# Kernel optimization log

Hardware: AMD Instinct MI355X
Metric: run time of the kernel (lower is better)

Reference implementation:

```python
import jax, jax.numpy as jnp
import numpy as np

B, T, D, H = 16, 4096, 256, 512  # batch, seq_len, ninputs, nhiddens


def setup_inputs() -> dict:
    key = jax.random.key(0)
    k_x, k_ih, k_hh, k_b, k_bn = jax.random.split(key, 5)
    s = 1.0 / np.sqrt(H)
    xs = jax.random.normal(k_x, (B, T, D), dtype=jnp.float32)
    W_ih = jax.random.uniform(k_ih, (3 * H, D), minval=-s, maxval=s, dtype=jnp.float32)
    W_hh = jax.random.uniform(k_hh, (3 * H, H), minval=-s, maxval=s, dtype=jnp.float32)
    b = jax.random.uniform(k_b, (3 * H,), minval=-s, maxval=s, dtype=jnp.float32)
    b_n = jax.random.uniform(k_bn, (H,), minval=-s, maxval=s, dtype=jnp.float32)
    return {"xs": xs, "W_ih": W_ih, "W_hh": W_hh, "b": b, "b_n": b_n}


def _gru_scan(xs, W_ih, W_hh, b, b_n):
    # Precompute all input-side gates with one big GEMM: (B, T, 3H)
    igates = jnp.einsum('btd,gd->btg', xs, W_ih) + b

    def step(h, ig):
        # h: (B, H), ig: (B, 3H)
        hg = h @ W_hh.T  # (B, 3H)
        i_r, i_z, i_n = jnp.split(ig, 3, axis=-1)
        h_r, h_z, h_n = jnp.split(hg, 3, axis=-1)
        r = jax.nn.sigmoid(i_r + h_r)   # reset gate
        z = jax.nn.sigmoid(i_z + h_z)   # update gate (equinox 'inp')
        n = jnp.tanh(i_n + r * (h_n + b_n))
        h_new = n + z * (h - n)         # equinox: new + inp * (hidden - new)
        return h_new, h_new

    h0 = jnp.zeros((xs.shape[0], b_n.shape[0]), dtype=xs.dtype)
    _, ys = jax.lax.scan(step, h0, jnp.swapaxes(igates, 0, 1))  # (T, B, H)
    return jnp.swapaxes(ys, 0, 1)  # (B, T, H)


def reference(xs, W_ih, W_hh, b, b_n):
    # CellLayer('gru', 'deer') computes the exact GRU recurrence over time
    # (DEER's fixed point equals the sequential evaluation).
    return _gru_scan(xs, W_ih, W_hh, b, b_n)
```

## Files before the change

### kernel.cpp

```cpp
#include <hip/hip_runtime.h>
#include <stdint.h>
#include <stddef.h>

#define B_ 16
#define T_ 4096
#define D_ 256
#define H_ 512
#define G3_ 1536

#define OFF_IG   ((size_t)0)
#define OFF_WT   ((size_t)201326592)
#define OFF_MB   ((size_t)202899456)
#define WS_NEED  ((size_t)203161600)

typedef _Float16 h2_t __attribute__((ext_vector_type(2)));

#if defined(__has_builtin)
#if __has_builtin(__builtin_amdgcn_fdot2)
#define HAVE_FDOT2 1
#endif
#endif

__device__ __forceinline__ float fdot2f(uint32_t w, uint32_t h, float acc) {
  union { uint32_t u; h2_t v; } a, b;
  a.u = w; b.u = h;
#ifdef HAVE_FDOT2
  return __builtin_amdgcn_fdot2(a.v, b.v, acc, false);
#else
  return fmaf((float)a.v.x, (float)b.v.x, fmaf((float)a.v.y, (float)b.v.y, acc));
#endif
}

__device__ __forceinline__ uint32_t packh2(float a, float b) {
  union { h2_t v; uint32_t u; } x;
  x.v.x = (_Float16)a; x.v.y = (_Float16)b;
  return x.u;
}

__device__ __forceinline__ uint32_t f16bits(float a) {
  union { _Float16 h; uint16_t u; } x;
  x.h = (_Float16)a;
  return (uint32_t)x.u;
}

__device__ __forceinline__ float h2f(uint16_t u) {
  union { _Float16 h; uint16_t u; } x;
  x.u = u;
  return (float)x.h;
}

__device__ __forceinline__ float sigmoidf_(float x) {
  return 1.0f / (1.0f + __expf(-x));
}

__device__ __forceinline__ float tanhf_(float x) {
  x = fminf(fmaxf(x, -15.0f), 15.0f);
  float e = __expf(-2.0f * x);
  return (1.0f - e) / (1.0f + e);
}

__global__ void __launch_bounds__(256) wt_kernel(const float* __restrict__ W, float4* __restrict__ Wt4) {
  int idx = blockIdx.x * 256 + threadIdx.x;
  if (idx >= G3_ * 64) return;
  int g = idx % G3_;
  int d4 = idx / G3_;
  float4 v = *(const float4*)(W + (size_t)g * D_ + 4 * d4);
  Wt4[(size_t)d4 * G3_ + g] = v;
}

__global__ void __launch_bounds__(256) ig_kernel(const float* __restrict__ xs,
                                                 const float* __restrict__ Wt,
                                                 const float* __restrict__ bias,
                                                 _Float16* __restrict__ ig) {
  __shared__ float xls[16 * 256];
  const int m0 = blockIdx.x * 16;
  const int tid = threadIdx.x;

  const float4* xsrc = (const float4*)(xs + (size_t)m0 * D_);
  float4* xdst = (float4*)xls;
#pragma unroll
  for (int k = 0; k < 4; ++k) xdst[tid + 256 * k] = xsrc[tid + 256 * k];
  __syncthreads();

  float acc[6][16];
#pragma unroll
  for (int k = 0; k < 6; ++k)
#pragma unroll
    for (int m = 0; m < 16; ++m) acc[k][m] = 0.0f;

  const float4* Wt4 = (const float4*)Wt;
  const float4* lds4 = (const float4*)xls;

  for (int d4 = 0; d4 < 64; ++d4) {
    float4 w[6];
#pragma unroll
    for (int k = 0; k < 6; ++k) w[k] = Wt4[(size_t)d4 * G3_ + tid + 256 * k];
#pragma unroll
    for (int m = 0; m < 16; ++m) {
      float4 xv = lds4[m * 64 + d4];
#pragma unroll
      for (int k = 0; k < 6; ++k) {
        acc[k][m] = fmaf(w[k].x, xv.x, acc[k][m]);
        acc[k][m] = fmaf(w[k].y, xv.y, acc[k][m]);
        acc[k][m] = fmaf(w[k].z, xv.z, acc[k][m]);
        acc[k][m] = fmaf(w[k].w, xv.w, acc[k][m]);
      }
    }
  }

#pragma unroll
  for (int k = 0; k < 6; ++k) {
    float bb = bias[tid + 256 * k];
#pragma unroll
    for (int m = 0; m < 16; ++m) {
      ig[(size_t)(m0 + m) * G3_ + tid + 256 * k] = (_Float16)(acc[k][m] + bb);
    }
  }
}

__global__ void __launch_bounds__(256, 1) rec_kernel(const _Float16* __restrict__ ig,
                                                     const float* __restrict__ Whh,
                                                     const float* __restrict__ bn,
                                                     uint32_t* __restrict__ mb,
                                                     float* __restrict__ out) {
  const int wg = blockIdx.x;
  const int b = wg >> 3;
  const int sub = wg & 7;
  const int tid = threadIdx.x;
  const int q = tid & 3;
  const int cl = tid >> 2;
  const int j = sub * 64 + cl;

  uint32_t wr[64], wz[64], wn[64];
  {
    const float4* s0 = (const float4*)(Whh + (size_t)j * H_ + q * 128);
    const float4* s1 = (const float4*)(Whh + (size_t)(j + H_) * H_ + q * 128);
    const float4* s2 = (const float4*)(Whh + (size_t)(j + 2 * H_) * H_ + q * 128);
#pragma unroll
    for (int i = 0; i < 32; ++i) {
      float4 v0 = s0[i]; wr[2 * i] = packh2(v0.x, v0.y); wr[2 * i + 1] = packh2(v0.z, v0.w);
      float4 v1 = s1[i]; wz[2 * i] = packh2(v1.x, v1.y); wz[2 * i + 1] = packh2(v1.z, v1.w);
      float4 v2 = s2[i]; wn[2 * i] = packh2(v2.x, v2.y); wn[2 * i + 1] = packh2(v2.z, v2.w);
    }
  }
  const float bnj = bn[j];

  __shared__ uint32_t hl[4 * 68];
  for (int i = tid; i < 4 * 68; i += 256) hl[i] = 0;
  __syncthreads();

  float hprev = 0.0f;

  const size_t mb_bc = ((size_t)b * 8 + sub) * 512;
  const size_t par_stride = (size_t)B_ * 8 * 512;
  const size_t dst0 = ((size_t)b * 8 + q) * 512 + (size_t)j;
  const size_t dst1 = ((size_t)b * 8 + (q + 4)) * 512 + (size_t)j;

  const uint16_t* ig16 = (const uint16_t*)ig;
  size_t igbase = (size_t)b * T_ * G3_;

  uint16_t cr = ig16[igbase + j];
  uint16_t cz = ig16[igbase + j + H_];
  uint16_t cn = ig16[igbase + j + 2 * H_];

  for (int t = 0; t < T_; ++t) {
    uint16_t nr = 0, nz = 0, nn_ = 0;
    if (t + 1 < T_) {
      const size_t nb = igbase + G3_;
      nr = ig16[nb + j];
      nz = ig16[nb + j + H_];
      nn_ = ig16[nb + j + 2 * H_];
    }

    if (t > 0) {
      const uint32_t* pb = mb + (size_t)(t & 1) * par_stride + mb_bc;
      const int k0 = 2 * tid;
      const uint32_t want = (uint32_t)t;
      uint32_t v0 = 0, v1 = 0;
      bool d0 = false, d1 = false;
      int guard = 0;
      for (;;) {
        uint32_t a0 = 0, a1 = 0;
        if (!d0) a0 = __hip_atomic_load(&pb[k0], __ATOMIC_RELAXED, __HIP_MEMORY_SCOPE_AGENT);
        if (!d1) a1 = __hip_atomic_load(&pb[k0 + 1], __ATOMIC_RELAXED, __HIP_MEMORY_SCOPE_AGENT);
        if (!d0 && (a0 >> 16) == want) { v0 = a0; d0 = true; }
        if (!d1 && (a1 >> 16) == want) { v1 = a1; d1 = true; }
        if (d0 && d1) break;
        if (++guard > 65536) {
          if (!d0) v0 = 0x7C00u;
          if (!d1) v1 = 0x7C00u;
          break;
        }
      }
      hl[(tid >> 6) * 68 + (tid & 63)] = (v0 & 0xFFFFu) | (v1 << 16);
      __syncthreads();
    }

    float ar0 = 0.0f, az0 = 0.0f, an0 = 0.0f;
    float ar1 = 0.0f, az1 = 0.0f, an1 = 0.0f;
    const uint4* hq = (const uint4*)(&hl[q * 68]);
#pragma unroll
    for (int i = 0; i < 8; ++i) {
      uint4 hv = hq[i];
      ar0 = fdot2f(wr[4 * i + 0], hv.x, ar0); az0 = fdot2f(wz[4 * i + 0], hv.x, az0); an0 = fdot2f(wn[4 * i + 0], hv.x, an0);
      ar0 = fdot2f(wr[4 * i + 1], hv.y, ar0); az0 = fdot2f(wz[4 * i + 1], hv.y, az0); an0 = fdot2f(wn[4 * i + 1], hv.y, an0);
      ar0 = fdot2f(wr[4 * i + 2], hv.z, ar0); az0 = fdot2f(wz[4 * i + 2], hv.z, az0); an0 = fdot2f(wn[4 * i + 2], hv.z, an0);
      ar0 = fdot2f(wr[4 * i + 3], hv.w, ar0); az0 = fdot2f(wz[4 * i + 3], hv.w, az0); an0 = fdot2f(wn[4 * i + 3], hv.w, an0);
    }
#pragma unroll
    for (int i = 8; i < 16; ++i) {
      uint4 hv = hq[i];
      ar1 = fdot2f(wr[4 * i + 0], hv.x, ar1); az1 = fdot2f(wz[4 * i + 0], hv.x, az1); an1 = fdot2f(wn[4 * i + 0], hv.x, an1);
      ar1 = fdot2f(wr[4 * i + 1], hv.y, ar1); az1 = fdot2f(wz[4 * i + 1], hv.y, az1); an1 = fdot2f(wn[4 * i + 1], hv.y, an1);
      ar1 = fdot2f(wr[4 * i + 2], hv.z, ar1); az1 = fdot2f(wz[4 * i + 2], hv.z, az1); an1 = fdot2f(wn[4 * i + 2], hv.z, an1);
      ar1 = fdot2f(wr[4 * i + 3], hv.w, ar1); az1 = fdot2f(wz[4 * i + 3], hv.w, an1 == an1 ? az1 : az1); an1 = fdot2f(wn[4 * i + 3], hv.w, an1);
    }
    __syncthreads();

    float ar = ar0 + ar1, az = az0 + az1, an = an0 + an1;
    ar += __shfl_xor(ar, 1); ar += __shfl_xor(ar, 2);
    az += __shfl_xor(az, 1); az += __shfl_xor(az, 2);
    an += __shfl_xor(an, 1); an += __shfl_xor(an, 2);

    const float igr = h2f(cr), igz = h2f(cz), ign = h2f(cn);
    const float r = sigmoidf_(igr + ar);
    const float z = sigmoidf_(igz + az);
    const float n = tanhf_(ign + r * (an + bnj));
    const float hnew = n + z * (hprev - n);
    hprev = hnew;

    const uint32_t wv = ((uint32_t)(t + 1) << 16) | f16bits(hnew);
    uint32_t* nbuf = mb + (size_t)((t + 1) & 1) * par_stride;
    __hip_atomic_store(&nbuf[dst0], wv, __ATOMIC_RELAXED, __HIP_MEMORY_SCOPE_AGENT);
    __hip_atomic_store(&nbuf[dst1], wv, __ATOMIC_RELAXED, __HIP_MEMORY_SCOPE_AGENT);

    if (q == 0) {
      out[((size_t)b * T_ + t) * H_ + j] = hnew;
    }

    cr = nr; cz = nz; cn = nn_;
    igbase += G3_;
  }
}

__global__ void __launch_bounds__(512) naive_kernel(const float* __restrict__ xs,
                                                    const float* __restrict__ Wih,
                                                    const float* __restrict__ Whh,
                                                    const float* __restrict__ bias,
                                                    const float* __restrict__ bn,
                                                    float* __restrict__ out) {
  const int b = blockIdx.x;
  const int j = threadIdx.x;
  __shared__ float h[H_];
  __shared__ float xr[D_];
  h[j] = 0.0f;
  __syncthreads();
  for (int t = 0; t < T_; ++t) {
    if (j < D_) xr[j] = xs[((size_t)b * T_ + t) * D_ + j];
    __syncthreads();
    float a[2];
#pragma unroll
    for (int g = 0; g < 2; ++g) {
      const int row = j + g * H_;
      float s = bias[row];
      const float* wi = Wih + (size_t)row * D_;
      for (int d = 0; d < D_; ++d) s = fmaf(wi[d], xr[d], s);
      const float* wh = Whh + (size_t)row * H_;
      for (int k = 0; k < H_; ++k) s = fmaf(wh[k], h[k], s);
      a[g] = s;
    }
    const float r = sigmoidf_(a[0]);
    const float z = sigmoidf_(a[1]);
    float i_n = bias[j + 2 * H_];
    {
      const float* wi = Wih + (size_t)(j + 2 * H_) * D_;
      for (int d = 0; d < D_; ++d) i_n = fmaf(wi[d], xr[d], i_n);
    }
    float h_n = 0.0f;
    {
      const float* wh = Whh + (size_t)(j + 2 * H_) * H_;
      for (int k = 0; k < H_; ++k) h_n = fmaf(wh[k], h[k], h_n);
    }
    const float nn = tanhf_(i_n + r * (h_n + bn[j]));
    const float hnew = nn + z * (h[j] - nn);
    __syncthreads();
    h[j] = hnew;
    out[((size_t)b * T_ + t) * H_ + j] = hnew;
  }
}

extern "C" void kernel_launch(void* const* d_in, const int* in_sizes, int n_in,
                              void* d_out, int out_size, void* d_ws, size_t ws_size,
                              hipStream_t stream) {
  const float* xs  = (const float*)d_in[0];
  const float* Wih = (const float*)d_in[1];
  const float* Whh = (const float*)d_in[2];
  const float* bia = (const float*)d_in[3];
  const float* bnp = (const float*)d_in[4];
  float* out = (float*)d_out;

  if (ws_size >= WS_NEED) {
    char* ws = (char*)d_ws;
    _Float16* igp = (_Float16*)(ws + OFF_IG);
    float* wtp = (float*)(ws + OFF_WT);
    uint32_t* mbp = (uint32_t*)(ws + OFF_MB);

    hipMemsetAsync(mbp, 0, 2 * B_ * 8 * 512 * sizeof(uint32_t), stream);

    wt_kernel<<<dim3(384), dim3(256), 0, stream>>>(Wih, (float4*)wtp);
    ig_kernel<<<dim3((B_ * T_) / 16), dim3(256), 0, stream>>>(xs, wtp, bia, igp);
    rec_kernel<<<dim3(128), dim3(256), 0, stream>>>(igp, Whh, bnp, mbp, out);
  } else {
    naive_kernel<<<dim3(B_), dim3(H_), 0, stream>>>(xs, Wih, Whh, bia, bnp, out);
  }
}
```

Baseline: 8.927 ms.

## Use sc0 polling loads, double-buffer shared h, remap workgroups across XCDs

The spin-wait on the per-step mailbox now uses inline-asm global loads with the sc0 cache bit instead of agent-scope atomic loads, with a fallback to the old atomic loop if polling exceeds a bound. Shared hidden-state staging is double-buffered by step parity, which removes one __syncthreads per timestep. Workgroup-to-(batch, sub) mapping is permuted so the eight slices of one batch land on the same XCD under round-robin dispatch, keeping mailbox traffic within one L2. The risks are relying on sc0 loads for cross-workgroup coherence and the single-barrier ordering.

```diff
diff --git a/kernel.cpp b/kernel.cpp
--- a/kernel.cpp
+++ b/kernel.cpp
@@ -59,6 +59,16 @@
   return (1.0f - e) / (1.0f + e);
 }
 
+__device__ __forceinline__ void load2_sc0(const uint32_t* p0, const uint32_t* p1,
+                                          uint32_t& a0, uint32_t& a1) {
+  asm volatile("global_load_dword %0, %2, off sc0\n\t"
+               "global_load_dword %1, %3, off sc0\n\t"
+               "s_waitcnt vmcnt(0)"
+               : "=&v"(a0), "=&v"(a1)
+               : "v"(p0), "v"(p1)
+               : "memory");
+}
+
 __global__ void __launch_bounds__(256) wt_kernel(const float* __restrict__ W, float4* __restrict__ Wt4) {
   int idx = blockIdx.x * 256 + threadIdx.x;
   if (idx >= G3_ * 64) return;
@@ -124,8 +134,10 @@
                                                      uint32_t* __restrict__ mb,
                                                      float* __restrict__ out) {
   const int wg = blockIdx.x;
-  const int b = wg >> 3;
-  const int sub = wg & 7;
+  const int c = wg & 7;
+  const int m_ = wg >> 3;
+  const int b = c + 8 * (m_ & 1);
+  const int sub = m_ >> 1;
   const int tid = threadIdx.x;
   const int q = tid & 3;
   const int cl = tid >> 2;
@@ -145,60 +157,72 @@
   }
   const float bnj = bn[j];
 
-  __shared__ uint32_t hl[4 * 68];
-  for (int i = tid; i < 4 * 68; i += 256) hl[i] = 0;
+  __shared__ uint32_t hl[2][4 * 68];
+  for (int i = tid; i < 2 * 4 * 68; i += 256) ((uint32_t*)hl)[i] = 0;
   __syncthreads();
 
   float hprev = 0.0f;
-
+  bool fast = true;
+
+  const size_t par_stride = (size_t)B_ * 8 * 512;
   const size_t mb_bc = ((size_t)b * 8 + sub) * 512;
-  const size_t par_stride = (size_t)B_ * 8 * 512;
   const size_t dst0 = ((size_t)b * 8 + q) * 512 + (size_t)j;
   const size_t dst1 = ((size_t)b * 8 + (q + 4)) * 512 + (size_t)j;
 
   const uint16_t* ig16 = (const uint16_t*)ig;
   size_t igbase = (size_t)b * T_ * G3_;
-
   uint16_t cr = ig16[igbase + j];
   uint16_t cz = ig16[igbase + j + H_];
   uint16_t cn = ig16[igbase + j + 2 * H_];
 
   for (int t = 0; t < T_; ++t) {
-    uint16_t nr = 0, nz = 0, nn_ = 0;
+    uint16_t nr = 0, nz = 0, nn2 = 0;
     if (t + 1 < T_) {
       const size_t nb = igbase + G3_;
       nr = ig16[nb + j];
       nz = ig16[nb + j + H_];
-      nn_ = ig16[nb + j + 2 * H_];
+      nn2 = ig16[nb + j + 2 * H_];
     }
 
     if (t > 0) {
-      const uint32_t* pb = mb + (size_t)(t & 1) * par_stride + mb_bc;
+      uint32_t* pb = mb + (size_t)(t & 1) * par_stride + mb_bc;
       const int k0 = 2 * tid;
       const uint32_t want = (uint32_t)t;
       uint32_t v0 = 0, v1 = 0;
       bool d0 = false, d1 = false;
-      int guard = 0;
-      for (;;) {
-        uint32_t a0 = 0, a1 = 0;
-        if (!d0) a0 = __hip_atomic_load(&pb[k0], __ATOMIC_RELAXED, __HIP_MEMORY_SCOPE_AGENT);
-        if (!d1) a1 = __hip_atomic_load(&pb[k0 + 1], __ATOMIC_RELAXED, __HIP_MEMORY_SCOPE_AGENT);
-        if (!d0 && (a0 >> 16) == want) { v0 = a0; d0 = true; }
-        if (!d1 && (a1 >> 16) == want) { v1 = a1; d1 = true; }
-        if (d0 && d1) break;
-        if (++guard > 65536) {
-          if (!d0) v0 = 0x7C00u;
-          if (!d1) v1 = 0x7C00u;
-          break;
+
+      if (fast) {
+        for (int g = 0; g < 4096; ++g) {
+          uint32_t a0, a1;
+          load2_sc0(&pb[k0], &pb[k0 + 1], a0, a1);
+          if (!d0 && (a0 >> 16) == want) { v0 = a0; d0 = true; }
+          if (!d1 && (a1 >> 16) == want) { v1 = a1; d1 = true; }
+          if (d0 && d1) break;
+        }
+        if (!(d0 && d1)) fast = false;
+      }
+      if (!(d0 && d1)) {
+        int guard = 0;
+        for (;;) {
+          uint32_t a0 = __hip_atomic_load(&pb[k0], __ATOMIC_RELAXED, __HIP_MEMORY_SCOPE_AGENT);
+          uint32_t a1 = __hip_atomic_load(&pb[k0 + 1], __ATOMIC_RELAXED, __HIP_MEMORY_SCOPE_AGENT);
+          if (!d0 && (a0 >> 16) == want) { v0 = a0; d0 = true; }
+          if (!d1 && (a1 >> 16) == want) { v1 = a1; d1 = true; }
+          if (d0 && d1) break;
+          if (++guard > (1 << 20)) {
+            if (!d0) v0 = 0x7C00u;
+            if (!d1) v1 = 0x7C00u;
+            break;
+          }
         }
       }
-      hl[(tid >> 6) * 68 + (tid & 63)] = (v0 & 0xFFFFu) | (v1 << 16);
-      __syncthreads();
-    }
-
+      hl[t & 1][(tid >> 6) * 68 + (tid & 63)] = (v0 & 0xFFFFu) | (v1 << 16);
+    }
+    __syncthreads();
+
+    const uint4* hq = (const uint4*)(&hl[t & 1][q * 68]);
     float ar0 = 0.0f, az0 = 0.0f, an0 = 0.0f;
     float ar1 = 0.0f, az1 = 0.0f, an1 = 0.0f;
-    const uint4* hq = (const uint4*)(&hl[q * 68]);
 #pragma unroll
     for (int i = 0; i < 8; ++i) {
       uint4 hv = hq[i];
@@ -213,9 +237,8 @@
       ar1 = fdot2f(wr[4 * i + 0], hv.x, ar1); az1 = fdot2f(wz[4 * i + 0], hv.x, az1); an1 = fdot2f(wn[4 * i + 0], hv.x, an1);
       ar1 = fdot2f(wr[4 * i + 1], hv.y, ar1); az1 = fdot2f(wz[4 * i + 1], hv.y, az1); an1 = fdot2f(wn[4 * i + 1], hv.y, an1);
       ar1 = fdot2f(wr[4 * i + 2], hv.z, ar1); az1 = fdot2f(wz[4 * i + 2], hv.z, az1); an1 = fdot2f(wn[4 * i + 2], hv.z, an1);
-      ar1 = fdot2f(wr[4 * i + 3], hv.w, ar1); az1 = fdot2f(wz[4 * i + 3], hv.w, an1 == an1 ? az1 : az1); an1 = fdot2f(wn[4 * i + 3], hv.w, an1);
-    }
-    __syncthreads();
+      ar1 = fdot2f(wr[4 * i + 3], hv.w, ar1); az1 = fdot2f(wz[4 * i + 3], hv.w, az1); an1 = fdot2f(wn[4 * i + 3], hv.w, an1);
+    }
 
     float ar = ar0 + ar1, az = az0 + az1, an = an0 + an1;
     ar += __shfl_xor(ar, 1); ar += __shfl_xor(ar, 2);
@@ -238,7 +261,7 @@
       out[((size_t)b * T_ + t) * H_ + j] = hnew;
     }
 
-    cr = nr; cz = nz; cn = nn_;
+    cr = nr; cz = nz; cn = nn2;
     igbase += G3_;
   }
 }
@@ -262,12 +285,12 @@
 #pragma unroll
     for (int g = 0; g < 2; ++g) {
       const int row = j + g * H_;
-      float s = bias[row];
+      float ssum = bias[row];
       const float* wi = Wih + (size_t)row * D_;
-      for (int d = 0; d < D_; ++d) s = fmaf(wi[d], xr[d], s);
+      for (int d = 0; d < D_; ++d) ssum = fmaf(wi[d], xr[d], ssum);
       const float* wh = Whh + (size_t)row * H_;
-      for (int k = 0; k < H_; ++k) s = fmaf(wh[k], h[k], s);
-      a[g] = s;
+      for (int kk = 0; kk < H_; ++kk) ssum = fmaf(wh[kk], h[kk], ssum);
+      a[g] = ssum;
     }
     const float r = sigmoidf_(a[0]);
     const float z = sigmoidf_(a[1]);
@@ -279,7 +302,7 @@
     float h_n = 0.0f;
     {
       const float* wh = Whh + (size_t)(j + 2 * H_) * H_;
-      for (int k = 0; k < H_; ++k) h_n = fmaf(wh[k], h[k], h_n);
+      for (int kk = 0; kk < H_; ++kk) h_n = fmaf(wh[kk], h[kk], h_n);
     }
     const float nn = tanhf_(i_n + r * (h_n + bn[j]));
     const float hnew = nn + z * (h[j] - nn);
```

Result: slower. 12.67 ms (+42.0%).
